# Kernel optimization log

Hardware: AMD Instinct MI355X
Metric: run time of the kernel (lower is better)

Reference implementation:

```python
import jax, jax.numpy as jnp
import numpy as np

N, E, CIN, CHID, DIM, KS = 6000, 192000, 32, 64, 3, 5
K = KS ** DIM          # 125 total spline kernel weights
S = 2 ** DIM           # 8 nonzero linear B-spline basis products per edge


def spline_conv(x, edge_index, pseudo, W, root, bias):
    """SplineConv, degree-1 open B-spline, mean aggregation, root weight + bias.
    x: [N, Cin], edge_index: [2, E], pseudo: [E, DIM] in [0,1],
    W: [K, Cin, Cout], root: [Cin, Cout], bias: [Cout].
    """
    src, dst = edge_index[0], edge_index[1]
    cin = x.shape[1]
    # open spline: KS-1 intervals over [0,1]
    u = pseudo * (KS - 1)                               # [E, DIM]
    i0 = jnp.clip(jnp.floor(u), 0, KS - 2).astype(jnp.int32)
    frac = u - i0                                       # [E, DIM]
    bits = (jnp.arange(S)[:, None] >> jnp.arange(DIM)[None, :]) & 1   # [S, DIM]
    strides = KS ** jnp.arange(DIM - 1, -1, -1)         # row-major flattening
    idx = jnp.sum((i0[:, None, :] + bits[None, :, :]) * strides, axis=-1)  # [E, S]
    basis = jnp.prod(jnp.where(bits[None, :, :] == 1,
                               frac[:, None, :], 1.0 - frac[:, None, :]), axis=-1)  # [E, S]
    x_j = x[src]                                        # gather: [E, Cin]
    vals = (basis[..., None] * x_j[:, None, :]).reshape(E * S, cin)
    keys = (dst[:, None] * K + idx).reshape(E * S)
    # bucket basis-weighted source features per (dst node, kernel index)
    T = jax.ops.segment_sum(vals, keys, num_segments=N * K).reshape(N, K, cin)
    out = jnp.einsum('nki,kio->no', T, W)               # [N, Cout]
    deg = jax.ops.segment_sum(jnp.ones((E,), jnp.float32), dst, num_segments=N)
    out = out / jnp.maximum(deg, 1.0)[:, None]          # mean aggregation
    return out + x @ root + bias


def _conv_params(key, cin):
    k1, k2 = jax.random.split(key)
    w_scale = 1.0 / np.sqrt(cin * S)
    W = jax.random.normal(k1, (K, cin, CHID), jnp.float32) * w_scale
    root = jax.random.normal(k2, (cin, CHID), jnp.float32) * (1.0 / np.sqrt(cin))
    b = jnp.zeros((CHID,), jnp.float32)
    return W, root, b


def setup_inputs() -> dict:
    key = jax.random.key(0)
    ks = jax.random.split(key, 10)
    inp = {
        'x': jax.random.normal(ks[0], (N, CIN), jnp.float32),
        'hidden': jax.random.normal(ks[1], (N, CHID), jnp.float32),
        'edge_index': jax.random.randint(ks[2], (2, E), 0, N, dtype=jnp.int32),
        'edge_attr': jax.random.uniform(ks[3], (E, DIM), jnp.float32),
    }
    for i, (name, cin) in enumerate([('xr', CIN), ('hr', CHID), ('xz', CIN),
                                     ('hz', CHID), ('xn', CIN), ('hn', CHID)]):
        W, root, b = _conv_params(ks[4 + i], cin)
        inp[f'W_{name}'] = W
        inp[f'root_{name}'] = root
        inp[f'b_{name}'] = b
    return inp


def reference(x, hidden, edge_index, edge_attr,
              W_xr, root_xr, b_xr, W_hr, root_hr, b_hr,
              W_xz, root_xz, b_xz, W_hz, root_hz, b_hz,
              W_xn, root_xn, b_xn, W_hn, root_hn, b_hn):
    hr_out = spline_conv(hidden, edge_index, edge_attr, W_hr, root_hr, b_hr)
    r = jax.nn.sigmoid(spline_conv(x, edge_index, edge_attr, W_xr, root_xr, b_xr) + hr_out)
    z = jax.nn.sigmoid(spline_conv(x, edge_index, edge_attr, W_xz, root_xz, b_xz)
                       + spline_conv(hidden, edge_index, edge_attr, W_hz, root_hz, b_hz))
    # NOTE: the original torch forward reuses self.hr (not self.hn) here; replicated faithfully.
    n = jnp.tanh(spline_conv(x, edge_index, edge_attr, W_xn, root_xn, b_xn) + r * hr_out)
    h_new = (1.0 - z) * n + z * hidden
    return h_new
```

## Files before the change

### kernel.cpp

```cpp
#include <hip/hip_runtime.h>
#include <math.h>

#define NN_   6000
#define EE_   192000
#define CIN_  32
#define CHID_ 64
#define KK_   125
#define EB_   32
#define CH1_  4
#define CH2_  8
#define CPB_  16

static __device__ __forceinline__ unsigned short f2bf(float f) {
    unsigned int u = __builtin_bit_cast(unsigned int, f);
    u += 0x7fff + ((u >> 16) & 1);
    return (unsigned short)(u >> 16);
}
static __device__ __forceinline__ float bf2f(unsigned short h) {
    unsigned int u = ((unsigned int)h) << 16;
    return __builtin_bit_cast(float, u);
}

#define PK1_ (192 * KK_ * CIN_)
#define PK2_ (128 * KK_ * CHID_)
#define CB_  ((EE_ + 255) / 256)
__global__ __launch_bounds__(256) void count_pack_kernel(
    const int* __restrict__ ei, int* __restrict__ deg,
    const float* __restrict__ W_xr, const float* __restrict__ W_xz,
    const float* __restrict__ W_xn, const float* __restrict__ W_hr,
    const float* __restrict__ W_hz,
    unsigned short* __restrict__ B1t, unsigned short* __restrict__ B2t)
{
    const int b = blockIdx.x;
    if (b < CB_) {
        int e = b * 256 + threadIdx.x;
        if (e < EE_) atomicAdd(&deg[ei[EE_ + e]], 1);
        return;
    }
    int gid = (b - CB_) * 256 + threadIdx.x;
    if (gid < PK1_) {
        int n  = gid / (KK_ * CIN_);
        int kk = gid % (KK_ * CIN_);
        int conv = n >> 6, o = n & 63;
        const float* W = (conv == 0) ? W_xr : ((conv == 1) ? W_xz : W_xn);
        B1t[gid] = f2bf(W[(size_t)kk * 64 + o]);
    } else if (gid < PK1_ + PK2_) {
        int g2 = gid - PK1_;
        int n  = g2 / (KK_ * CHID_);
        int kk = g2 % (KK_ * CHID_);
        int conv = n >> 6, o = n & 63;
        const float* W = (conv == 0) ? W_hr : W_hz;
        B2t[g2] = f2bf(W[(size_t)kk * 64 + o]);
    }
}

__global__ __launch_bounds__(1024) void scan_kernel(
    const int* __restrict__ deg, int* __restrict__ offs, int* __restrict__ cursor)
{
    __shared__ int part[1024];
    const int tid = threadIdx.x;
    const int CH = (NN_ + 1023) / 1024;
    const int base = tid * CH;
    int loc[CH];
    int s = 0;
#pragma unroll
    for (int i = 0; i < CH; ++i) {
        int v = (base + i < NN_) ? deg[base + i] : 0;
        loc[i] = s; s += v;
    }
    part[tid] = s;
    __syncthreads();
    for (int off = 1; off < 1024; off <<= 1) {
        int v = (tid >= off) ? part[tid - off] : 0;
        __syncthreads();
        part[tid] += v;
        __syncthreads();
    }
    const int pre = (tid > 0) ? part[tid - 1] : 0;
#pragma unroll
    for (int i = 0; i < CH; ++i) {
        if (base + i < NN_) {
            offs[base + i]   = pre + loc[i];
            cursor[base + i] = pre + loc[i];
        }
    }
    if (tid == 1023) offs[NN_] = part[1023];
}

__global__ __launch_bounds__(256) void prep_kernel(
    const int* __restrict__ ei, const float* __restrict__ attr,
    int* __restrict__ cursor, float4* __restrict__ meta_s, int* __restrict__ src_s)
{
    int e = blockIdx.x * 256 + threadIdx.x;
    if (e >= EE_) return;
    const int dst = ei[EE_ + e];
    const int p   = atomicAdd(&cursor[dst], 1);
    float f[3]; int i0[3];
#pragma unroll
    for (int d = 0; d < 3; ++d) {
        float u  = attr[e * 3 + d] * 4.0f;
        float fl = floorf(u);
        fl = fminf(fmaxf(fl, 0.0f), 3.0f);
        i0[d] = (int)fl;
        f[d]  = u - fl;
    }
    meta_s[p] = make_float4(f[0], f[1], f[2],
        __int_as_float(i0[0] * 25 + i0[1] * 5 + i0[2]));
    src_s[p] = ei[e];
}

template<int C>
__global__ __launch_bounds__(256) void build_T_kernel(
    const float4* __restrict__ meta_s, const int* __restrict__ src_s,
    const float* __restrict__ feat, const int* __restrict__ offs,
    unsigned short* __restrict__ Tb)
{
    constexpr int MP  = 40;
    constexpr int CT  = C / 16;
    constexpr int CPT = C / 8;
    using bf16x8 = __attribute__((ext_vector_type(8))) short;
    using f32x4  = __attribute__((ext_vector_type(4))) float;

    __shared__ __align__(16) unsigned short Mt [128 * MP];
    __shared__ __align__(16) unsigned short fbT[C   * MP];
    __shared__ int s_src[EB_];

    const int tid  = threadIdx.x;
    const int wave = tid >> 6;
    const int lane = tid & 63;
    const int quad = lane >> 4;
    const int l16  = lane & 15;
    const int node = blockIdx.x;

    for (int i = tid; i < C * MP / 8; i += 256)
        ((uint4*)fbT)[i] = make_uint4(0u, 0u, 0u, 0u);

    const int j0 = offs[node], j1 = offs[node + 1];

    f32x4 acc[2][CT];
#pragma unroll
    for (int t = 0; t < 2; ++t)
#pragma unroll
        for (int ct = 0; ct < CT; ++ct) acc[t][ct] = (f32x4){0.f, 0.f, 0.f, 0.f};

    for (int jb = j0; jb < j1; jb += EB_) {
        const int m = min(EB_, j1 - jb);

        __syncthreads();
        for (int i = tid; i < 128 * MP / 8; i += 256)
            ((uint4*)Mt)[i] = make_uint4(0u, 0u, 0u, 0u);
        if (tid < m) s_src[tid] = src_s[jb + tid];
        __syncthreads();

        if (tid < m) {
            const float4 mt = meta_s[jb + tid];
            const int base = __float_as_int(mt.w);
            const float f0 = mt.x, f1 = mt.y, f2 = mt.z;
            const float g0 = 1.f - f0, g1 = 1.f - f1, g2 = 1.f - f2;
            const float bb[8] = {g0*g1*g2, f0*g1*g2, g0*f1*g2, f0*f1*g2,
                                 g0*g1*f2, f0*g1*f2, g0*f1*f2, f0*f1*f2};
            const int oc[8] = {0, 25, 5, 30, 1, 26, 6, 31};
#pragma unroll
            for (int s = 0; s < 8; ++s)
                Mt[(base + oc[s]) * MP + tid] = f2bf(bb[s]);
        }
        {
            const int e = tid >> 3, cg = (tid & 7) * CPT;
            if (e < m) {
                const float* fr = &feat[(size_t)s_src[e] * C + cg];
#pragma unroll
                for (int c4 = 0; c4 < CPT; c4 += 4) {
                    float4 v = *(const float4*)(fr + c4);
                    fbT[(cg + c4 + 0) * MP + e] = f2bf(v.x);
                    fbT[(cg + c4 + 1) * MP + e] = f2bf(v.y);
                    fbT[(cg + c4 + 2) * MP + e] = f2bf(v.z);
                    fbT[(cg + c4 + 3) * MP + e] = f2bf(v.w);
                }
            }
        }
        __syncthreads();

        bf16x8 a0 = *(const bf16x8*)&Mt[((wave * 2 + 0) * 16 + l16) * MP + quad * 8];
        bf16x8 a1 = *(const bf16x8*)&Mt[((wave * 2 + 1) * 16 + l16) * MP + quad * 8];
#pragma unroll
        for (int ct = 0; ct < CT; ++ct) {
            bf16x8 b = *(const bf16x8*)&fbT[(ct * 16 + l16) * MP + quad * 8];
            acc[0][ct] = __builtin_amdgcn_mfma_f32_16x16x32_bf16(a0, b, acc[0][ct], 0, 0, 0);
            acc[1][ct] = __builtin_amdgcn_mfma_f32_16x16x32_bf16(a1, b, acc[1][ct], 0, 0, 0);
        }
    }

    unsigned short* To = Tb + (size_t)node * (KK_ * C);
#pragma unroll
    for (int t = 0; t < 2; ++t) {
        const int rbase = (wave * 2 + t) * 16 + quad * 4;
#pragma unroll
        for (int ct = 0; ct < CT; ++ct) {
#pragma unroll
            for (int r = 0; r < 4; ++r) {
                const int R = rbase + r;
                if (R < KK_) To[R * C + ct * 16 + l16] = f2bf(acc[t][ct][r]);
            }
        }
    }
}

template<int NT, int NTF, int CPB>
static __device__ __forceinline__ void gemm_body(
    unsigned char* arena,
    const unsigned short* __restrict__ A, const unsigned short* __restrict__ Bt,
    unsigned short* __restrict__ P, int M, int Kd, int chunk, int zhalf)
{
    constexpr int SPC   = 2;
    constexpr int COLS  = SPC * 32;
    constexpr int BP    = COLS + 8;
    constexpr int NFRAG = NT / 16;
    constexpr int CSP   = NT + 8;
    unsigned short (*Bs)[BP] = (unsigned short(*)[BP])arena;

    using bf16x8 = __attribute__((ext_vector_type(8))) short;
    using f32x4  = __attribute__((ext_vector_type(4))) float;

    const int tid  = threadIdx.x;
    const int wave = tid >> 6;
    const int lane = tid & 63;
    const int quad = lane >> 4;
    const int l16  = lane & 15;
    const int m0   = blockIdx.x * 64;
    const unsigned short* Bp = Bt + (size_t)zhalf * NT * Kd;

    const int  arow   = m0 + wave * 16 + l16;
    const bool avalid = arow < M;
    const unsigned short* Ap = A + (size_t)(avalid ? arow : 0) * Kd;

    f32x4 acc[NFRAG];
#pragma unroll
    for (int f = 0; f < NFRAG; ++f) acc[f] = (f32x4){0.f, 0.f, 0.f, 0.f};

    for (int cc = 0; cc < CPB; ++cc) {
        const int k0 = (chunk * CPB + cc) * COLS;
        if (k0 >= Kd) break;
        const int ksz = min(Kd - k0, COLS);

        __syncthreads();

        constexpr int BUNITS = NT * COLS / 8;
        for (int u = tid; u < BUNITS; u += 256) {
            const int row = u / (COLS / 8);
            const int cq  = (u % (COLS / 8)) * 8;
            uint4 v = make_uint4(0u, 0u, 0u, 0u);
            if (cq < ksz) v = *(const uint4*)(Bp + (size_t)row * Kd + k0 + cq);
            *(uint4*)&Bs[row][cq] = v;
        }

        uint4 afr[SPC];
#pragma unroll
        for (int s = 0; s < SPC; ++s) {
            const int k = k0 + s * 32 + quad * 8;
            afr[s] = (avalid && k < Kd) ? *(const uint4*)(Ap + k)
                                        : make_uint4(0u, 0u, 0u, 0u);
        }

        __syncthreads();

#pragma unroll
        for (int s = 0; s < SPC; ++s) {
            bf16x8 af = __builtin_bit_cast(bf16x8, afr[s]);
#pragma unroll
            for (int f = 0; f < NFRAG; ++f) {
                bf16x8 bfv = *(bf16x8*)&Bs[f * 16 + l16][s * 32 + quad * 8];
                acc[f] = __builtin_amdgcn_mfma_f32_16x16x32_bf16(af, bfv, acc[f], 0, 0, 0);
            }
        }
    }

    __syncthreads();
    unsigned short* Cs = (unsigned short*)arena;
    const int rbase = wave * 16 + quad * 4;
#pragma unroll
    for (int f = 0; f < NFRAG; ++f) {
        const int col = f * 16 + l16;
#pragma unroll
        for (int r = 0; r < 4; ++r)
            Cs[(rbase + r) * CSP + col] = f2bf(acc[f][r]);
    }
    __syncthreads();
    unsigned short* Pc = P + ((size_t)chunk * M + m0) * NTF + zhalf * NT;
    constexpr int UNITS = 64 * NT / 8;
    for (int u = tid; u < UNITS; u += 256) {
        const int row = (u * 8) / NT, col = (u * 8) % NT;
        if (m0 + row < M)
            *(uint4*)&Pc[(size_t)row * NTF + col] = *(const uint4*)&Cs[row * CSP + col];
    }
}

__global__ __launch_bounds__(256) void gemm_all_kernel(
    const unsigned short* __restrict__ Tx, const unsigned short* __restrict__ B1t,
    unsigned short* __restrict__ P1,
    const unsigned short* __restrict__ Th, const unsigned short* __restrict__ B2t,
    unsigned short* __restrict__ P2)
{
    __shared__ __align__(16) unsigned char arena[128 * 72 * 2];
    const int y = blockIdx.y;
    if (y < CH2_) {
        gemm_body<128, 128, CPB_>(arena, Th, B2t, P2, NN_, KK_ * CHID_, y, 0);
    } else {
        const int g = y - CH2_;
        gemm_body<96, 192, CPB_>(arena, Tx, B1t, P1, NN_, KK_ * CIN_, g >> 1, g & 1);
    }
}

__global__ __launch_bounds__(256) void epilogue_kernel(
    const unsigned short* __restrict__ P1, const unsigned short* __restrict__ P2,
    const int* __restrict__ offs,
    const float* __restrict__ x, const float* __restrict__ hidden,
    const float* __restrict__ root_xr, const float* __restrict__ root_hr,
    const float* __restrict__ root_xz, const float* __restrict__ root_hz,
    const float* __restrict__ root_xn,
    const float* __restrict__ b_xr, const float* __restrict__ b_hr,
    const float* __restrict__ b_xz, const float* __restrict__ b_hz,
    const float* __restrict__ b_xn,
    float* __restrict__ out)
{
    __shared__ float xsh[4][32];
    __shared__ float hsh[4][64];
    const int w = threadIdx.x >> 6;
    const int o = threadIdx.x & 63;
    const int m = blockIdx.x * 4 + w;
    if (m >= NN_) return;

    if (o < 32) xsh[w][o] = x[(size_t)m * 32 + o];
    const float hval = hidden[(size_t)m * 64 + o];
    hsh[w][o] = hval;

    float axr = 0.f, axz = 0.f, axn = 0.f;
#pragma unroll
    for (int c = 0; c < CH1_; ++c) {
        const unsigned short* p = P1 + ((size_t)c * NN_ + m) * 192;
        axr += bf2f(p[o]); axz += bf2f(p[64 + o]); axn += bf2f(p[128 + o]);
    }
    float ahr = 0.f, ahz = 0.f;
#pragma unroll
    for (int c = 0; c < CH2_; ++c) {
        const unsigned short* p = P2 + ((size_t)c * NN_ + m) * 128;
        ahr += bf2f(p[o]); ahz += bf2f(p[64 + o]);
    }

    const int   dg   = offs[m + 1] - offs[m];
    const float dinv = 1.0f / fmaxf((float)dg, 1.0f);
    axr *= dinv; axz *= dinv; axn *= dinv; ahr *= dinv; ahz *= dinv;

    float sxr = 0.f, sxz = 0.f, sxn = 0.f;
#pragma unroll
    for (int c = 0; c < CIN_; ++c) {
        float xv = xsh[w][c];
        sxr += xv * root_xr[c * 64 + o];
        sxz += xv * root_xz[c * 64 + o];
        sxn += xv * root_xn[c * 64 + o];
    }
    float shr = 0.f, shz = 0.f;
#pragma unroll
    for (int c = 0; c < CHID_; ++c) {
        float hv = hsh[w][c];
        shr += hv * root_hr[c * 64 + o];
        shz += hv * root_hz[c * 64 + o];
    }

    const float conv_xr = axr + sxr + b_xr[o];
    const float conv_xz = axz + sxz + b_xz[o];
    const float conv_xn = axn + sxn + b_xn[o];
    const float hr_out  = ahr + shr + b_hr[o];
    const float conv_hz = ahz + shz + b_hz[o];

    const float rg = 1.0f / (1.0f + expf(-(conv_xr + hr_out)));
    const float zg = 1.0f / (1.0f + expf(-(conv_xz + conv_hz)));
    const float ng = tanhf(conv_xn + rg * hr_out);
    out[(size_t)m * 64 + o] = (1.0f - zg) * ng + zg * hval;
}

extern "C" void kernel_launch(void* const* d_in, const int* in_sizes, int n_in,
                              void* d_out, int out_size, void* d_ws, size_t ws_size,
                              hipStream_t stream)
{
    const float* x       = (const float*)d_in[0];
    const float* hidden  = (const float*)d_in[1];
    const int*   ei      = (const int*)  d_in[2];
    const float* attr    = (const float*)d_in[3];
    const float* W_xr    = (const float*)d_in[4];
    const float* root_xr = (const float*)d_in[5];
    const float* b_xr    = (const float*)d_in[6];
    const float* W_hr    = (const float*)d_in[7];
    const float* root_hr = (const float*)d_in[8];
    const float* b_hr    = (const float*)d_in[9];
    const float* W_xz    = (const float*)d_in[10];
    const float* root_xz = (const float*)d_in[11];
    const float* b_xz    = (const float*)d_in[12];
    const float* W_hz    = (const float*)d_in[13];
    const float* root_hz = (const float*)d_in[14];
    const float* b_hz    = (const float*)d_in[15];
    const float* W_xn    = (const float*)d_in[16];
    const float* root_xn = (const float*)d_in[17];
    const float* b_xn    = (const float*)d_in[18];
    float* out = (float*)d_out;

    char* w = (char*)d_ws;
    unsigned short* Tx  = (unsigned short*)w; w += (size_t)NN_ * KK_ * CIN_  * 2;
    unsigned short* Th  = (unsigned short*)w; w += (size_t)NN_ * KK_ * CHID_ * 2;
    unsigned short* B1t = (unsigned short*)w; w += (size_t)192 * KK_ * CIN_  * 2;
    unsigned short* B2t = (unsigned short*)w; w += (size_t)128 * KK_ * CHID_ * 2;
    unsigned short* P1  = (unsigned short*)w; w += (size_t)CH1_ * NN_ * 192 * 2;
    unsigned short* P2  = (unsigned short*)w; w += (size_t)CH2_ * NN_ * 128 * 2;
    float4* meta_s = (float4*)w; w += (size_t)EE_ * 16;
    int* src_s  = (int*)w;   w += (size_t)EE_ * 4;
    int* deg    = (int*)w;   w += (size_t)NN_ * 4;
    int* offs   = (int*)w;   w += (size_t)(NN_ + 4) * 4;
    int* cursor = (int*)w;   w += (size_t)NN_ * 4;

    const int MT = (NN_ + 63) / 64;

    hipMemsetAsync(deg, 0, (size_t)NN_ * 4, stream);

    const int PACKB = (PK1_ + PK2_ + 255) / 256;
    count_pack_kernel<<<CB_ + PACKB, 256, 0, stream>>>(
        ei, deg, W_xr, W_xz, W_xn, W_hr, W_hz, B1t, B2t);

    scan_kernel<<<1, 1024, 0, stream>>>(deg, offs, cursor);
    prep_kernel<<<(EE_ + 255) / 256, 256, 0, stream>>>(ei, attr, cursor, meta_s, src_s);

    build_T_kernel<CHID_><<<NN_, 256, 0, stream>>>(meta_s, src_s, hidden, offs, Th);
    build_T_kernel<CIN_><<<NN_, 256, 0, stream>>>(meta_s, src_s, x, offs, Tx);

    gemm_all_kernel<<<dim3(MT, CH2_ + 2 * CH1_), 256, 0, stream>>>(
        Tx, B1t, P1, Th, B2t, P2);

    epilogue_kernel<<<(NN_ + 3) / 4, 256, 0, stream>>>(
        P1, P2, offs, x, hidden,
        root_xr, root_hr, root_xz, root_hz, root_xn,
        b_xr, b_hr, b_xz, b_hz, b_xn, out);
}
```

Measured before the change: 251.8 us.

## Enlarge GEMM M-tile to 192 with double-buffered direct-to-LDS B staging

The GEMM block now covers 192 rows instead of 64, so each wave computes three 16-row fragments and reuses every B fragment read from LDS across them. B tiles are loaded with global_load_lds into two XOR-swizzled LDS buffers, and the next chunk's B and A loads are issued before the current chunk's MFMAs, overlapping memory with compute and dropping one barrier per iteration. This raises register pressure (acc is 3x larger) and cuts the grid to about a third as many blocks, which could reduce occupancy and load balance. The output write-back is done in three 64-row passes through LDS.

```diff
diff --git a/kernel.cpp b/kernel.cpp
--- a/kernel.cpp
+++ b/kernel.cpp
@@ -10,6 +10,7 @@
 #define CH1_  4
 #define CH2_  8
 #define CPB_  16
+#define MTILE_ 192
 
 static __device__ __forceinline__ unsigned short f2bf(float f) {
     unsigned int u = __builtin_bit_cast(unsigned int, f);
@@ -211,86 +212,126 @@
     const unsigned short* __restrict__ A, const unsigned short* __restrict__ Bt,
     unsigned short* __restrict__ P, int M, int Kd, int chunk, int zhalf)
 {
-    constexpr int SPC   = 2;
-    constexpr int COLS  = SPC * 32;
-    constexpr int BP    = COLS + 8;
-    constexpr int NFRAG = NT / 16;
-    constexpr int CSP   = NT + 8;
-    unsigned short (*Bs)[BP] = (unsigned short(*)[BP])arena;
+    constexpr int COLS   = 64;
+    constexpr int RF     = 3;
+    constexpr int NFRAG  = NT / 16;
+    constexpr int CSP    = NT + 8;
+    constexpr int BUNITS = NT * COLS / 8;
 
     using bf16x8 = __attribute__((ext_vector_type(8))) short;
     using f32x4  = __attribute__((ext_vector_type(4))) float;
+
+    unsigned short* Bs0 = (unsigned short*)arena;
+    unsigned short* Bs1 = (unsigned short*)(arena + NT * COLS * 2);
 
     const int tid  = threadIdx.x;
     const int wave = tid >> 6;
     const int lane = tid & 63;
     const int quad = lane >> 4;
     const int l16  = lane & 15;
-    const int m0   = blockIdx.x * 64;
+    const int m0   = blockIdx.x * MTILE_;
     const unsigned short* Bp = Bt + (size_t)zhalf * NT * Kd;
-
-    const int  arow   = m0 + wave * 16 + l16;
-    const bool avalid = arow < M;
-    const unsigned short* Ap = A + (size_t)(avalid ? arow : 0) * Kd;
-
-    f32x4 acc[NFRAG];
-#pragma unroll
-    for (int f = 0; f < NFRAG; ++f) acc[f] = (f32x4){0.f, 0.f, 0.f, 0.f};
-
-    for (int cc = 0; cc < CPB; ++cc) {
-        const int k0 = (chunk * CPB + cc) * COLS;
-        if (k0 >= Kd) break;
-        const int ksz = min(Kd - k0, COLS);
-
-        __syncthreads();
-
-        constexpr int BUNITS = NT * COLS / 8;
-        for (int u = tid; u < BUNITS; u += 256) {
-            const int row = u / (COLS / 8);
-            const int cq  = (u % (COLS / 8)) * 8;
-            uint4 v = make_uint4(0u, 0u, 0u, 0u);
-            if (cq < ksz) v = *(const uint4*)(Bp + (size_t)row * Kd + k0 + cq);
-            *(uint4*)&Bs[row][cq] = v;
-        }
-
-        uint4 afr[SPC];
-#pragma unroll
-        for (int s = 0; s < SPC; ++s) {
-            const int k = k0 + s * 32 + quad * 8;
-            afr[s] = (avalid && k < Kd) ? *(const uint4*)(Ap + k)
-                                        : make_uint4(0u, 0u, 0u, 0u);
-        }
-
-        __syncthreads();
-
-#pragma unroll
-        for (int s = 0; s < SPC; ++s) {
-            bf16x8 af = __builtin_bit_cast(bf16x8, afr[s]);
+    const int kbase = chunk * CPB * COLS;
+    const int ccmax = min(CPB, (Kd - kbase + COLS - 1) / COLS);
+
+    bool avalid[RF]; const unsigned short* Ap[RF];
+#pragma unroll
+    for (int t = 0; t < RF; ++t) {
+        const int ar = m0 + (wave * RF + t) * 16 + l16;
+        avalid[t] = ar < M;
+        Ap[t] = A + (size_t)(avalid[t] ? ar : 0) * Kd;
+    }
+
+    f32x4 acc[RF][NFRAG];
+#pragma unroll
+    for (int t = 0; t < RF; ++t)
+#pragma unroll
+        for (int f = 0; f < NFRAG; ++f) acc[t][f] = (f32x4){0.f, 0.f, 0.f, 0.f};
+
+    uint4 afC[RF][2], afN[RF][2];
+
+    auto STAGE = [&](int cc, unsigned short* B) {
+        const int k0 = kbase + cc * COLS;
+#pragma unroll
+        for (int i = 0; i < BUNITS / 256; ++i) {
+            const int u   = tid + i * 256;
+            const int row = u >> 3;
+            const int blk = (u & 7) ^ (row & 7);
+            const unsigned short* g = Bp + (size_t)row * Kd + k0 + blk * 8;
+            __builtin_amdgcn_global_load_lds(
+                (const __attribute__((address_space(1))) void*)g,
+                (__attribute__((address_space(3))) void*)(B + u * 8),
+                16, 0, 0);
+        }
+    };
+    auto LOADA = [&](int cc, uint4 (&af)[RF][2]) {
+        const int k0 = kbase + cc * COLS;
+#pragma unroll
+        for (int t = 0; t < RF; ++t)
+#pragma unroll
+            for (int s = 0; s < 2; ++s) {
+                const int k = k0 + s * 32 + quad * 8;
+                af[t][s] = (avalid[t] && k < Kd) ? *(const uint4*)(Ap[t] + k)
+                                                 : make_uint4(0u, 0u, 0u, 0u);
+            }
+    };
+
+    STAGE(0, Bs0);
+    LOADA(0, afC);
+    __syncthreads();
+
+    for (int cc = 0; cc < ccmax; ++cc) {
+        unsigned short* bc = (cc & 1) ? Bs1 : Bs0;
+        unsigned short* bn = (cc & 1) ? Bs0 : Bs1;
+        const bool havenext = (cc + 1 < ccmax);
+        if (havenext) { STAGE(cc + 1, bn); LOADA(cc + 1, afN); }
+#pragma unroll
+        for (int s = 0; s < 2; ++s)
 #pragma unroll
             for (int f = 0; f < NFRAG; ++f) {
-                bf16x8 bfv = *(bf16x8*)&Bs[f * 16 + l16][s * 32 + quad * 8];
-                acc[f] = __builtin_amdgcn_mfma_f32_16x16x32_bf16(af, bfv, acc[f], 0, 0, 0);
-            }
-        }
-    }
-
-    __syncthreads();
+                bf16x8 bv = *(const bf16x8*)
+                    &bc[(f * 16 + l16) * COLS + (((s * 4 + quad) ^ (l16 & 7)) * 8)];
+#pragma unroll
+                for (int t = 0; t < RF; ++t)
+                    acc[t][f] = __builtin_amdgcn_mfma_f32_16x16x32_bf16(
+                        __builtin_bit_cast(bf16x8, afC[t][s]), bv, acc[t][f], 0, 0, 0);
+            }
+        __syncthreads();
+        if (havenext) {
+#pragma unroll
+            for (int t = 0; t < RF; ++t) {
+                afC[t][0] = afN[t][0]; afC[t][1] = afN[t][1];
+            }
+        }
+    }
+
     unsigned short* Cs = (unsigned short*)arena;
-    const int rbase = wave * 16 + quad * 4;
-#pragma unroll
-    for (int f = 0; f < NFRAG; ++f) {
-        const int col = f * 16 + l16;
-#pragma unroll
-        for (int r = 0; r < 4; ++r)
-            Cs[(rbase + r) * CSP + col] = f2bf(acc[f][r]);
-    }
-    __syncthreads();
     unsigned short* Pc = P + ((size_t)chunk * M + m0) * NTF + zhalf * NT;
-    constexpr int UNITS = 64 * NT / 8;
-    for (int u = tid; u < UNITS; u += 256) {
-        const int row = (u * 8) / NT, col = (u * 8) % NT;
-        if (m0 + row < M)
-            *(uint4*)&Pc[(size_t)row * NTF + col] = *(const uint4*)&Cs[row * CSP + col];
+#pragma unroll
+    for (int p = 0; p < 3; ++p) {
+        __syncthreads();
+#pragma unroll
+        for (int t = 0; t < RF; ++t) {
+            const int fr = wave * RF + t;
+            if ((fr >> 2) == p) {
+                const int rb = (fr & 3) * 16 + quad * 4;
+#pragma unroll
+                for (int f = 0; f < NFRAG; ++f) {
+                    const int col = f * 16 + l16;
+#pragma unroll
+                    for (int r = 0; r < 4; ++r)
+                        Cs[(rb + r) * CSP + col] = f2bf(acc[t][f][r]);
+                }
+            }
+        }
+        __syncthreads();
+        constexpr int UNITS = 64 * NT / 8;
+        for (int u = tid; u < UNITS; u += 256) {
+            const int row = (u * 8) / NT, col = (u * 8) % NT;
+            if (m0 + p * 64 + row < M)
+                *(uint4*)&Pc[(size_t)(p * 64 + row) * NTF + col] =
+                    *(const uint4*)&Cs[row * CSP + col];
+        }
     }
 }
 
@@ -300,7 +341,7 @@
     const unsigned short* __restrict__ Th, const unsigned short* __restrict__ B2t,
     unsigned short* __restrict__ P2)
 {
-    __shared__ __align__(16) unsigned char arena[128 * 72 * 2];
+    __shared__ __align__(16) unsigned char arena[2 * 128 * 64 * 2];
     const int y = blockIdx.y;
     if (y < CH2_) {
         gemm_body<128, 128, CPB_>(arena, Th, B2t, P2, NN_, KK_ * CHID_, y, 0);
@@ -416,7 +457,7 @@
     int* offs   = (int*)w;   w += (size_t)(NN_ + 4) * 4;
     int* cursor = (int*)w;   w += (size_t)NN_ * 4;
 
-    const int MT = (NN_ + 63) / 64;
+    const int MT = (NN_ + MTILE_ - 1) / MTILE_;
 
     hipMemsetAsync(deg, 0, (size_t)NN_ * 4, stream);
 
```

New measurement: 250.2 us. About the same (-0.6%).
